# Performance work log

Measured on AMD Instinct MI355X. Metric: run time of the kernel, lower is better.

The kernel has to match this reference:

```python
import jax, jax.numpy as jnp
import numpy as np

N = 10000          # nodes
E = 200000         # edges (avg degree 20)
LAT = 128          # latent dim
NEXP = 8           # experts
NTYPE = 95         # atom types (hard-coded 95x0e in module)
M0, M1, M2 = 128, 64, 32          # node/out irreps muls for l=0,1,2 (dim 480)
E0, E1, E2 = 64, 32, 16           # edge irreps muls (dim 240)
C0, C1, C2 = M0 + E0, M1 + E1, M2 + E2   # concat channels per l
T0 = M0 + M1 + M2                 # gate-input scalars: 128 scalars + 96 gates
AVG_NEIGH = 20.0


def setup_inputs() -> dict:
    key = jax.random.key(0)
    ks = jax.random.split(key, 32)
    r = lambda i, sh: jax.random.normal(ks[i], sh, dtype=jnp.float32)
    return {
        "latents": r(0, (E, LAT)),
        "node_features": r(1, (N, M0 + 3 * M1 + 5 * M2)),
        "edge_features": r(2, (E, E0 + 3 * E1 + 5 * E2)),
        "edge_vector": r(3, (E, 3)),
        "mole_globals": r(4, (LAT,)),
        "wigner_D1": r(5, (E, 3, 3)),
        "wigner_D2": r(6, (E, 5, 5)),
        "node_onehot": jax.nn.one_hot(jax.random.randint(ks[7], (N,), 0, NTYPE), NTYPE, dtype=jnp.float32),
        "Wg": r(8, (LAT, NEXP)),
        "Wm": r(9, (LAT, NEXP)),
        "W0_e": r(10, (NEXP, C0, T0)), "W0_s": r(11, (C0, T0)),
        "W1_e": r(12, (NEXP, C1, M1)), "W1_s": r(13, (C1, M1)),
        "W2_e": r(14, (NEXP, C2, M2)), "W2_s": r(15, (C2, M2)),
        "Wp0": r(16, (M0, M0)), "bp0": jnp.zeros((M0,), jnp.float32),
        "Wp1": r(17, (M1, M1)), "Wp2": r(18, (M2, M2)),
        "Wenv": r(19, (LAT, M0 + M1 + M2)),
        "Woh0": r(20, (M0, NTYPE)), "Woh1": r(21, (M1, NTYPE)), "Woh2": r(22, (M2, NTYPE)),
        "atom_type": jax.random.randint(ks[23], (N,), 0, NTYPE),
        "edge_index": jax.random.randint(ks[24], (2, E), 0, N),
        "active_edges": jnp.arange(E),
    }


def _mix(x, We, Ws, g):
    """Latent(expert)-conditioned per-l channel mixing: y = x @ (sum_e g_e W_e + W_shared).
    Loops over the small fixed expert count; never materializes per-edge weight matrices."""
    xm = x if x.ndim == 3 else x[:, :, None]           # [a, c, m]
    y = jnp.einsum('acm,co->aom', xm, Ws)
    for e in range(NEXP):
        y = y + g[:, e, None, None] * jnp.einsum('acm,co->aom', xm, We[e])
    y = y * float(1.0 / np.sqrt(xm.shape[1]))
    return y[:, :, 0] if x.ndim == 2 else y


def reference(latents, node_features, edge_features, edge_vector, mole_globals,
              wigner_D1, wigner_D2, node_onehot, Wg, Wm,
              W0_e, W0_s, W1_e, W1_s, W2_e, W2_s,
              Wp0, bp0, Wp1, Wp2, Wenv, Woh0, Woh1, Woh2,
              atom_type, edge_index, active_edges):
    edge_center = edge_index[0][active_edges]
    lat = latents[active_edges]
    # gather node features along edges, split irreps blocks
    xn = node_features[edge_center]                         # [Ea, 480]
    n0 = xn[:, :M0]
    n1 = xn[:, M0:M0 + 3 * M1].reshape(-1, M1, 3)
    n2 = xn[:, M0 + 3 * M1:].reshape(-1, M2, 5)
    e0 = edge_features[:, :E0]
    e1 = edge_features[:, E0:E0 + 3 * E1].reshape(-1, E1, 3)
    e2 = edge_features[:, E0 + 3 * E1:].reshape(-1, E2, 5)
    x0 = jnp.concatenate([n0, e0], axis=1)                  # [Ea, C0]
    x1 = jnp.concatenate([n1, e1], axis=1)                  # [Ea, C1, 3]
    x2 = jnp.concatenate([n2, e2], axis=1)                  # [Ea, C2, 5]
    # latent + molecular-global conditioned expert gates
    gates = jax.nn.softmax(lat @ Wg + mole_globals @ Wm, axis=-1)   # [Ea, NEXP]
    # SO(2)-style TP: rotate l>0 blocks into edge frame (Wigner-D), mix channels, rotate back
    x1r = jnp.einsum('amn,acn->acm', wigner_D1, x1)
    x2r = jnp.einsum('amn,acn->acm', wigner_D2, x2)
    t0 = _mix(x0, W0_e, W0_s, gates)                        # [Ea, T0]
    t1 = jnp.einsum('anm,aom->aon', wigner_D1, _mix(x1r, W1_e, W1_s, gates))
    t2 = jnp.einsum('anm,aom->aon', wigner_D2, _mix(x2r, W2_e, W2_s, gates))
    # Gate nonlinearity: silu scalars, sigmoid gates scale l>0 channels
    s = jax.nn.silu(t0[:, :M0])
    v1 = t1 * jax.nn.sigmoid(t0[:, M0:M0 + M1])[:, :, None]
    v2 = t2 * jax.nn.sigmoid(t0[:, M0 + M1:])[:, :, None]
    # lin_post: per-l equivariant linear (bias only on scalars), fan-in normalized
    s = s @ Wp0 * float(1.0 / np.sqrt(M0)) + bp0
    v1 = jnp.einsum('acm,co->aom', v1, Wp1) * float(1.0 / np.sqrt(M1))
    v2 = jnp.einsum('acm,co->aom', v2, Wp2) * float(1.0 / np.sqrt(M2))
    # E3ElementLinear: per-channel weights generated from latents
    w = lat @ Wenv * float(1.0 / np.sqrt(LAT))              # [Ea, M0+M1+M2]
    s = s * w[:, :M0]
    v1 = v1 * w[:, M0:M0 + M1, None]
    v2 = v2 * w[:, M0 + M1:, None]
    # scatter-reduce messages to nodes, normalize by rsqrt(avg_num_neighbors)
    norm = float(1.0 / np.sqrt(AVG_NEIGH))
    o0 = jax.ops.segment_sum(s, edge_center, num_segments=N) * norm
    o1 = jax.ops.segment_sum(v1, edge_center, num_segments=N) * norm
    o2 = jax.ops.segment_sum(v2, edge_center, num_segments=N) * norm
    # residual blend (res_update_params=0 -> u=sigmoid(0)=0.5), identity residual
    u = 0.5
    c_old = float(1.0 / np.sqrt(u * u + 1.0))
    c_new = u * c_old
    h0 = c_old * node_features[:, :M0] + c_new * o0
    h1 = c_old * node_features[:, M0:M0 + 3 * M1].reshape(N, M1, 3) + c_new * o1
    h2 = c_old * node_features[:, M0 + 3 * M1:].reshape(N, M2, 5) + c_new * o2
    # layer-onehot 'uvu' weighted TP with 95x0e, fan-in normalized, added residually
    invs = float(1.0 / np.sqrt(NTYPE))
    h0 = h0 + h0 * (node_onehot @ Woh0.T) * invs
    h1 = h1 + h1 * (node_onehot @ Woh1.T)[:, :, None] * invs
    h2 = h2 + h2 * (node_onehot @ Woh2.T)[:, :, None] * invs
    return jnp.concatenate([h0, h1.reshape(N, 3 * M1), h2.reshape(N, 5 * M2)], axis=1)
```

## Files before the change

kernel.cpp:

```cpp
#include <hip/hip_runtime.h>
#include <math.h>

namespace {

typedef __attribute__((ext_vector_type(8))) short short8;
typedef __attribute__((ext_vector_type(4))) float f32x4;

constexpr int kN   = 10000;
constexpr int kE   = 200000;
constexpr int kNT  = 95;
constexpr int kNFD = 480;

__device__ __forceinline__ ushort bf(float f) {
  union { float f; uint u; } c; c.f = f;
  uint r = c.u + 0x7FFF + ((c.u >> 16) & 1);
  return (ushort)(r >> 16);
}
__device__ __forceinline__ float fb(ushort u) {
  union { uint u; float f; } c; c.u = ((uint)u) << 16;
  return c.f;
}
__device__ __forceinline__ uint pk2(float a, float b) {
  return (uint)bf(a) | ((uint)bf(b) << 16);
}

__device__ __forceinline__ void fastbar() {
  asm volatile("s_waitcnt lgkmcnt(0)" ::: "memory");
  __builtin_amdgcn_s_barrier();
}

__device__ __forceinline__ void packone(int u, const float* We, const float* Ws,
                                        int expStride, int Kreal, int Nstride,
                                        int Nreal, int NT, int NKp, ushort* d) {
  int i = u & 7;
  int lane = (u >> 3) & 63;
  int rest = u >> 9;
  int kc = rest % NKp; rest /= NKp;
  int nt = rest % NT;
  int e  = rest / NT;
  int k = kc*32 + (lane >> 4)*8 + i;
  int n = nt*16 + (lane & 15);
  float v = 0.f;
  if (k < Kreal && n < Nreal) {
    const float* s = (Ws != nullptr && e == 8) ? Ws : (We + (size_t)e*expStride);
    v = s[(size_t)k*Nstride + n];
  }
  d[u] = bf(v);
}

constexpr int PK0   = 0;
constexpr int PK1   = 442368;
constexpr int PK2   = 497664;
constexpr int PKENV = 516096;
constexpr int PKP0  = 544768;
constexpr int PKP1  = 561152;
constexpr int PKP2  = 565248;
constexpr int PKTOT = 566272;

__global__ __launch_bounds__(256)
void pack_k(const float* __restrict__ W0e, const float* __restrict__ W0s,
            const float* __restrict__ W1e, const float* __restrict__ W1s,
            const float* __restrict__ W2e, const float* __restrict__ W2s,
            const float* __restrict__ Wenv, const float* __restrict__ Wp0,
            const float* __restrict__ Wp1, const float* __restrict__ Wp2,
            ushort* __restrict__ dst) {
  int gid = blockIdx.x*256 + threadIdx.x;
  if (gid >= PKTOT) return;
  if (gid < PK1)        packone(gid - PK0,   W0e, W0s, 192*224, 192, 224, 224, 16, 6, dst + PK0);
  else if (gid < PK2)   packone(gid - PK1,   W1e, W1s, 96*64,    96,  64,  64,  4, 3, dst + PK1);
  else if (gid < PKENV) packone(gid - PK2,   W2e, W2s, 48*32,    48,  32,  32,  2, 2, dst + PK2);
  else if (gid < PKP0)  packone(gid - PKENV, Wenv, nullptr, 0,  128, 224, 224, 14, 4, dst + PKENV);
  else if (gid < PKP1)  packone(gid - PKP0,  Wp0, nullptr, 0,   128, 128, 128,  8, 4, dst + PKP0);
  else if (gid < PKP2)  packone(gid - PKP1,  Wp1, nullptr, 0,    64,  64,  64,  4, 2, dst + PKP1);
  else                  packone(gid - PKP2,  Wp2, nullptr, 0,    32,  32,  32,  2, 1, dst + PKP2);
}

__global__ __launch_bounds__(64)
void mgl_k(const float* __restrict__ mgv, const float* __restrict__ Wm,
           float* __restrict__ mgl) {
  int x = threadIdx.x;
  if (x < 8) {
    float s = 0.f;
    for (int l = 0; l < 128; ++l) s += mgv[l]*Wm[l*8 + x];
    mgl[x] = s;
  }
}

__global__ __launch_bounds__(256)
void hist_k(const int* __restrict__ eidx, const int* __restrict__ act,
            int* __restrict__ counts) {
  int e = blockIdx.x*256 + threadIdx.x;
  if (e < kE) atomicAdd(&counts[eidx[act[e]]], 1);
}

__global__ __launch_bounds__(256)
void scan_k(const int* __restrict__ counts, int* __restrict__ rowptr,
            int* __restrict__ cursor) {
  __shared__ int part[256];
  const int t = threadIdx.x;
  const int start = t*40;
  int local = 0;
  for (int i = 0; i < 40; ++i) {
    int idx = start + i;
    if (idx < kN) local += counts[idx];
  }
  part[t] = local;
  __syncthreads();
  for (int ofs = 1; ofs < 256; ofs <<= 1) {
    int v = (t >= ofs) ? part[t - ofs] : 0;
    __syncthreads();
    part[t] += v;
    __syncthreads();
  }
  int run = part[t] - local;
  for (int i = 0; i < 40; ++i) {
    int idx = start + i;
    if (idx < kN) {
      rowptr[idx] = run;
      cursor[idx] = run;
      run += counts[idx];
    }
  }
  if (t == 255) rowptr[kN] = run;
}

__global__ __launch_bounds__(256)
void scatter_k(const int* __restrict__ eidx, const int* __restrict__ act,
               int* __restrict__ cursor, int* __restrict__ elist) {
  int e = blockIdx.x*256 + threadIdx.x;
  if (e < kE) {
    int n = eidx[act[e]];
    int pos = atomicAdd(&cursor[n], 1);
    elist[pos] = e;
  }
}

__global__ __launch_bounds__(256)
void prep_k(const float* __restrict__ latents, const float* __restrict__ nodef,
            const float* __restrict__ edgef, const float* __restrict__ mgl,
            const float* __restrict__ D1, const float* __restrict__ D2,
            const float* __restrict__ Wg,
            const int* __restrict__ eidx, const int* __restrict__ act,
            float* __restrict__ coefg,
            ushort* __restrict__ x0, ushort* __restrict__ x1r,
            ushort* __restrict__ x2r) {
  __shared__ int aidl[32], cenl[32];
  const int tid = threadIdx.x;
  const int base = blockIdx.x*32;

  if (tid < 32) {
    int a = act[base + tid];
    aidl[tid] = a;
    cenl[tid] = eidx[a];
  }
  __syncthreads();

  {
    int e = tid >> 3, x = tid & 7;
    const float* lat = latents + (size_t)aidl[e]*128;
    float s = mgl[x];
    for (int l = 0; l < 128; ++l) s += lat[l]*Wg[l*8 + x];
    float mx = s;
    mx = fmaxf(mx, __shfl_xor(mx, 1));
    mx = fmaxf(mx, __shfl_xor(mx, 2));
    mx = fmaxf(mx, __shfl_xor(mx, 4));
    float ex = __expf(s - mx);
    float sm = ex;
    sm += __shfl_xor(sm, 1);
    sm += __shfl_xor(sm, 2);
    sm += __shfl_xor(sm, 4);
    size_t a = base + e;
    coefg[a*9 + x] = ex/sm;
    if (x == 0) coefg[a*9 + 8] = 1.f;
  }

  for (int u = tid; u < 32*24; u += 256) {
    int e = u/24, g = u - e*24;
    int c0 = g*8;
    size_t a = base + e;
    const float* s = (g < 16) ? (nodef + (size_t)cenl[e]*kNFD + c0)
                              : (edgef + a*240 + (c0 - 128));
    float4 f0 = *(const float4*)s;
    float4 f1 = *(const float4*)(s + 4);
    uint4 o;
    o.x = pk2(f0.x, f0.y); o.y = pk2(f0.z, f0.w);
    o.z = pk2(f1.x, f1.y); o.w = pk2(f1.z, f1.w);
    *(uint4*)(x0 + a*192 + c0) = o;
  }

  for (int u = tid; u < 32*36; u += 256) {
    int e = u/36, r = u - e*36;
    int mm = r/12, g = r - mm*12;
    int c0 = g*8;
    size_t a = base + e;
    const float* dd = D1 + a*9 + mm*3;
    const float* s = (g < 8) ? (nodef + (size_t)cenl[e]*kNFD + 128 + c0*3)
                             : (edgef + a*240 + 64 + (c0 - 64)*3);
    float ld[24];
    #pragma unroll
    for (int q = 0; q < 6; ++q)
      *(float4*)(ld + q*4) = *(const float4*)(s + q*4);
    float d0 = dd[0], d1 = dd[1], d2 = dd[2];
    float ov[8];
    #pragma unroll
    for (int j = 0; j < 8; ++j)
      ov[j] = d0*ld[3*j] + d1*ld[3*j + 1] + d2*ld[3*j + 2];
    uint4 o;
    o.x = pk2(ov[0], ov[1]); o.y = pk2(ov[2], ov[3]);
    o.z = pk2(ov[4], ov[5]); o.w = pk2(ov[6], ov[7]);
    *(uint4*)(x1r + (a*3 + mm)*96 + c0) = o;
  }

  for (int u = tid; u < 32*40; u += 256) {
    int e = u/40, r = u - e*40;
    int mm = r >> 3, g = r & 7;
    int c0 = g*8;
    size_t a = base + e;
    uint4 o = {0u,0u,0u,0u};
    if (g < 6) {
      const float* dd = D2 + a*25 + mm*5;
      const float* s = (g < 4) ? (nodef + (size_t)cenl[e]*kNFD + 320 + c0*5)
                               : (edgef + a*240 + 160 + (c0 - 32)*5);
      float ld[40];
      #pragma unroll
      for (int q = 0; q < 10; ++q)
        *(float4*)(ld + q*4) = *(const float4*)(s + q*4);
      float d0 = dd[0], d1 = dd[1], d2 = dd[2], d3 = dd[3], d4 = dd[4];
      float ov[8];
      #pragma unroll
      for (int j = 0; j < 8; ++j)
        ov[j] = d0*ld[5*j] + d1*ld[5*j+1] + d2*ld[5*j+2] + d3*ld[5*j+3] + d4*ld[5*j+4];
      o.x = pk2(ov[0], ov[1]); o.y = pk2(ov[2], ov[3]);
      o.z = pk2(ov[4], ov[5]); o.w = pk2(ov[6], ov[7]);
    }
    *(uint4*)(x2r + (a*5 + mm)*64 + c0) = o;
  }
}

constexpr int gemm_smbytes(int K1, int NK, int N, int NEXP) {
  int LDA = K1 + 8;
  int NT = N/16;
  int a = 128*LDA*2;
  int b = NT*NK*1024;
  int u = a > b ? a : b;
  return u + (NEXP > 1 ? 128*NEXP*4 : 0);
}

template<int DIV, int K1, int NK, int N, int NEXP, int EPI, bool AF32>
__global__ __launch_bounds__(512)
void gemm_k(const ushort* __restrict__ A, const float* __restrict__ Af,
            const int* __restrict__ ridx, int strideA,
            const ushort* __restrict__ Bpk, const float* __restrict__ coefg,
            int rowsReal, float norm,
            ushort* __restrict__ outbf, const float* __restrict__ bias,
            const ushort* __restrict__ wenvbf, int WCOL) {
  constexpr int NT  = N/16;
  constexpr int CTW = NT/2;
  constexpr int LDA = K1 + 8;
  constexpr int ABYTES = 128*LDA*2;
  constexpr int BBYTES = NT*NK*1024;
  constexpr int UNI = (ABYTES > BBYTES) ? ABYTES : BBYTES;

  extern __shared__ char smraw[];
  ushort* Asm = (ushort*)smraw;
  float* coefsm = (float*)(smraw + UNI);

  const int tid = threadIdx.x;
  const int row0 = blockIdx.x*128;

  constexpr int C8 = K1/8;
  for (int u = tid; u < 128*C8; u += 512) {
    int r = u / C8, c8 = u - r*C8;
    int gr = row0 + r;
    uint4 v = {0u,0u,0u,0u};
    if (gr < rowsReal) {
      if constexpr (AF32) {
        const float* s = Af + (size_t)(ridx ? ridx[gr] : gr)*strideA + c8*8;
        float4 f0 = *(const float4*)s;
        float4 f1 = *(const float4*)(s + 4);
        v.x = pk2(f0.x, f0.y); v.y = pk2(f0.z, f0.w);
        v.z = pk2(f1.x, f1.y); v.w = pk2(f1.z, f1.w);
      } else {
        v = *(const uint4*)(A + (size_t)gr*strideA + c8*8);
      }
    }
    *(uint4*)(&Asm[r*LDA + c8*8]) = v;
  }
  if constexpr (NEXP > 1) {
    for (int u = tid; u < 128*NEXP; u += 512) {
      int r = u / NEXP, e = u - r*NEXP;
      int a = (row0 + r)/DIV;
      coefsm[r*NEXP + e] = coefg[(size_t)a*NEXP + e];
    }
  }
  __syncthreads();

  const int lane = tid & 63, wid = tid >> 6;
  const int cg = wid & 1, rg = wid >> 1;
  const int rbase = rg*32;
  const int lrow = lane & 15, lkb = lane >> 4;

  short8 af[2][NK];
  #pragma unroll
  for (int rt = 0; rt < 2; ++rt)
    #pragma unroll
    for (int kc = 0; kc < NK; ++kc)
      af[rt][kc] = *(const short8*)(&Asm[(rbase + rt*16 + lrow)*LDA + kc*32 + lkb*8]);

  f32x4 acc[2][CTW];
  #pragma unroll
  for (int rt = 0; rt < 2; ++rt)
    #pragma unroll
    for (int ct = 0; ct < CTW; ++ct)
      acc[rt][ct] = f32x4{0.f,0.f,0.f,0.f};

  __syncthreads();

  union BU { uint4 u; short8 s; };
  uint4* Bsm4 = (uint4*)smraw;
  const uint4* Bg4 = (const uint4*)Bpk;

  for (int e = 0; e < NEXP; ++e) {
    for (int u = tid; u < NT*NK*64; u += 512)
      Bsm4[u] = Bg4[(size_t)e*(NT*NK*64) + u];
    __syncthreads();

    if constexpr (NEXP > 1) {
      float cf[2][4];
      #pragma unroll
      for (int rt = 0; rt < 2; ++rt)
        #pragma unroll
        for (int q = 0; q < 4; ++q)
          cf[rt][q] = coefsm[(rbase + rt*16 + lkb*4 + q)*NEXP + e];
      #pragma unroll
      for (int ct = 0; ct < CTW; ++ct) {
        int nt = cg*CTW + ct;
        f32x4 z[2];
        z[0] = f32x4{0.f,0.f,0.f,0.f};
        z[1] = f32x4{0.f,0.f,0.f,0.f};
        #pragma unroll
        for (int kc = 0; kc < NK; ++kc) {
          BU b; b.u = Bsm4[(nt*NK + kc)*64 + lane];
          z[0] = __builtin_amdgcn_mfma_f32_16x16x32_bf16(af[0][kc], b.s, z[0], 0, 0, 0);
          z[1] = __builtin_amdgcn_mfma_f32_16x16x32_bf16(af[1][kc], b.s, z[1], 0, 0, 0);
        }
        #pragma unroll
        for (int q = 0; q < 4; ++q) {
          acc[0][ct][q] += cf[0][q]*z[0][q];
          acc[1][ct][q] += cf[1][q]*z[1][q];
        }
      }
    } else {
      #pragma unroll
      for (int ct = 0; ct < CTW; ++ct) {
        int nt = cg*CTW + ct;
        #pragma unroll
        for (int kc = 0; kc < NK; ++kc) {
          BU b; b.u = Bsm4[(nt*NK + kc)*64 + lane];
          acc[0][ct] = __builtin_amdgcn_mfma_f32_16x16x32_bf16(af[0][kc], b.s, acc[0][ct], 0, 0, 0);
          acc[1][ct] = __builtin_amdgcn_mfma_f32_16x16x32_bf16(af[1][kc], b.s, acc[1][ct], 0, 0, 0);
        }
      }
    }
    __syncthreads();
  }

  #pragma unroll
  for (int rt = 0; rt < 2; ++rt) {
    #pragma unroll
    for (int ct = 0; ct < CTW; ++ct) {
      #pragma unroll
      for (int q = 0; q < 4; ++q) {
        int gr = row0 + rbase + rt*16 + lkb*4 + q;
        if (gr >= rowsReal) continue;
        int o = (cg*CTW + ct)*16 + lrow;
        float val = acc[rt][ct][q]*norm;
        if constexpr (EPI == 0) {
          outbf[(size_t)gr*N + o] = bf(val);
        } else if constexpr (EPI == 1) {
          float av = (o < 128) ? (val/(1.f + __expf(-val)))
                               : (1.f/(1.f + __expf(-val)));
          outbf[(size_t)gr*N + o] = bf(av);
        } else {
          int a = gr/DIV;
          if (bias != nullptr) val += bias[o];
          float w = fb(wenvbf[(size_t)a*224 + WCOL + o]);
          val *= w*0.22360679774997896f;
          outbf[(size_t)gr*N + o] = bf(val);
        }
      }
    }
  }
}

template<int L>
__global__ __launch_bounds__(512)
void pv_k(const ushort* __restrict__ y, const ushort* __restrict__ t0act,
          const float* __restrict__ Dm, const ushort* __restrict__ Bpk,
          int rowsReal, float norm, const ushort* __restrict__ wenvbf,
          ushort* __restrict__ peout) {
  constexpr int DIV = (L == 1) ? 3 : 5;
  constexpr int K1  = (L == 1) ? 64 : 32;
  constexpr int NK  = K1/32;
  constexpr int N   = K1;
  constexpr int NT  = N/16;
  constexpr int CTW = NT/2;
  constexpr int LDA = K1 + 8;
  constexpr int WCOL = (L == 1) ? 128 : 192;
  constexpr int DSTR = (L == 1) ? 9 : 25;
  constexpr int ABYTES = 128*LDA*2;
  constexpr int BBYTES = NT*NK*1024;
  constexpr int UNI = (ABYTES > BBYTES) ? ABYTES : BBYTES;

  extern __shared__ char smraw[];
  ushort* Asm = (ushort*)smraw;

  const int tid = threadIdx.x;
  const int row0 = blockIdx.x*128;

  constexpr int C8 = K1/8;
  for (int u = tid; u < 128*C8; u += 512) {
    int r = u / C8, c8 = u - r*C8;
    int c0 = c8*8;
    int gr = row0 + r;
    uint4 v = {0u,0u,0u,0u};
    if (gr < rowsReal) {
      int a = gr/DIV, n = gr - a*DIV;
      const float* dd = Dm + (size_t)a*DSTR + n*DIV;
      short8 gt = *(const short8*)(t0act + (size_t)a*224 + WCOL + c0);
      float ov[8];
      if constexpr (L == 1) {
        short8 m0 = *(const short8*)(y + ((size_t)a*3 + 0)*64 + c0);
        short8 m1 = *(const short8*)(y + ((size_t)a*3 + 1)*64 + c0);
        short8 m2 = *(const short8*)(y + ((size_t)a*3 + 2)*64 + c0);
        float d0 = dd[0], d1 = dd[1], d2 = dd[2];
        #pragma unroll
        for (int j = 0; j < 8; ++j) {
          float s = d0*fb((ushort)m0[j]) + d1*fb((ushort)m1[j]) + d2*fb((ushort)m2[j]);
          ov[j] = s*fb((ushort)gt[j]);
        }
      } else {
        short8 m0 = *(const short8*)(y + ((size_t)a*5 + 0)*32 + c0);
        short8 m1 = *(const short8*)(y + ((size_t)a*5 + 1)*32 + c0);
        short8 m2 = *(const short8*)(y + ((size_t)a*5 + 2)*32 + c0);
        short8 m3 = *(const short8*)(y + ((size_t)a*5 + 3)*32 + c0);
        short8 m4 = *(const short8*)(y + ((size_t)a*5 + 4)*32 + c0);
        float d0 = dd[0], d1 = dd[1], d2 = dd[2], d3 = dd[3], d4 = dd[4];
        #pragma unroll
        for (int j = 0; j < 8; ++j) {
          float s = d0*fb((ushort)m0[j]) + d1*fb((ushort)m1[j])
                  + d2*fb((ushort)m2[j]) + d3*fb((ushort)m3[j])
                  + d4*fb((ushort)m4[j]);
          ov[j] = s*fb((ushort)gt[j]);
        }
      }
      v.x = pk2(ov[0], ov[1]); v.y = pk2(ov[2], ov[3]);
      v.z = pk2(ov[4], ov[5]); v.w = pk2(ov[6], ov[7]);
    }
    *(uint4*)(&Asm[r*LDA + c0]) = v;
  }
  __syncthreads();

  const int lane = tid & 63, wid = tid >> 6;
  const int cg = wid & 1, rg = wid >> 1;
  const int rbase = rg*32;
  const int lrow = lane & 15, lkb = lane >> 4;

  short8 af[2][NK];
  #pragma unroll
  for (int rt = 0; rt < 2; ++rt)
    #pragma unroll
    for (int kc = 0; kc < NK; ++kc)
      af[rt][kc] = *(const short8*)(&Asm[(rbase + rt*16 + lrow)*LDA + kc*32 + lkb*8]);

  f32x4 acc[2][CTW];
  #pragma unroll
  for (int rt = 0; rt < 2; ++rt)
    #pragma unroll
    for (int ct = 0; ct < CTW; ++ct)
      acc[rt][ct] = f32x4{0.f,0.f,0.f,0.f};

  __syncthreads();

  union BU { uint4 u; short8 s; };
  uint4* Bsm4 = (uint4*)smraw;
  const uint4* Bg4 = (const uint4*)Bpk;

  for (int u = tid; u < NT*NK*64; u += 512)
    Bsm4[u] = Bg4[u];
  __syncthreads();

  #pragma unroll
  for (int ct = 0; ct < CTW; ++ct) {
    int nt = cg*CTW + ct;
    #pragma unroll
    for (int kc = 0; kc < NK; ++kc) {
      BU b; b.u = Bsm4[(nt*NK + kc)*64 + lane];
      acc[0][ct] = __builtin_amdgcn_mfma_f32_16x16x32_bf16(af[0][kc], b.s, acc[0][ct], 0, 0, 0);
      acc[1][ct] = __builtin_amdgcn_mfma_f32_16x16x32_bf16(af[1][kc], b.s, acc[1][ct], 0, 0, 0);
    }
  }

  #pragma unroll
  for (int rt = 0; rt < 2; ++rt) {
    #pragma unroll
    for (int ct = 0; ct < CTW; ++ct) {
      #pragma unroll
      for (int q = 0; q < 4; ++q) {
        int gr = row0 + rbase + rt*16 + lkb*4 + q;
        if (gr >= rowsReal) continue;
        int o = (cg*CTW + ct)*16 + lrow;
        int a = gr/DIV;
        float val = acc[rt][ct][q]*norm;
        float w = fb(wenvbf[(size_t)a*224 + WCOL + o]);
        val *= w*0.22360679774997896f;
        peout[(size_t)gr*N + o] = bf(val);
      }
    }
  }
}

constexpr int T0SMB = 55808;

template<int C>
__device__ __forceinline__ void t0_phase(int e, int tid, int lane, int cg,
                                         int rbase, int lkb,
                                         const short8 (&af)[2][6],
                                         f32x4 (&acc)[2][7],
                                         const float* coefsm,
                                         uint4* Bsm4, const uint4* Bg4,
                                         uint4& rg0, uint4& rg1, uint4& rg2) {
  fastbar();
  const bool hasNext = !(e == 8 && C == 3);
  if (hasNext) {
    int ne = e + (C == 3 ? 1 : 0);
    int nc = (C + 1) & 3;
    const uint4* s = Bg4 + (size_t)ne*6144 + (size_t)nc*1536;
    rg0 = s[tid]; rg1 = s[tid + 512]; rg2 = s[tid + 1024];
  }
  float cf[2][4];
  #pragma unroll
  for (int rt = 0; rt < 2; ++rt)
    #pragma unroll
    for (int q = 0; q < 4; ++q)
      cf[rt][q] = coefsm[(rbase + rt*16 + lkb*4 + q)*9 + e];
  union BU { uint4 u; short8 s; };
  const uint4* bb = Bsm4 + (C & 1)*1536;
  {
    f32x4 z0 = {0.f,0.f,0.f,0.f}, z1 = {0.f,0.f,0.f,0.f};
    #pragma unroll
    for (int kc = 0; kc < 6; ++kc) {
      BU b; b.u = bb[(cg*6 + kc)*64 + lane];
      z0 = __builtin_amdgcn_mfma_f32_16x16x32_bf16(af[0][kc], b.s, z0, 0, 0, 0);
      z1 = __builtin_amdgcn_mfma_f32_16x16x32_bf16(af[1][kc], b.s, z1, 0, 0, 0);
    }
    #pragma unroll
    for (int q = 0; q < 4; ++q) {
      acc[0][2*C][q] += cf[0][q]*z0[q];
      acc[1][2*C][q] += cf[1][q]*z1[q];
    }
  }
  if constexpr (2*C + 1 < 7) {
    f32x4 z0 = {0.f,0.f,0.f,0.f}, z1 = {0.f,0.f,0.f,0.f};
    #pragma unroll
    for (int kc = 0; kc < 6; ++kc) {
      BU b; b.u = bb[((2 + cg)*6 + kc)*64 + lane];
      z0 = __builtin_amdgcn_mfma_f32_16x16x32_bf16(af[0][kc], b.s, z0, 0, 0, 0);
      z1 = __builtin_amdgcn_mfma_f32_16x16x32_bf16(af[1][kc], b.s, z1, 0, 0, 0);
    }
    #pragma unroll
    for (int q = 0; q < 4; ++q) {
      acc[0][2*C + 1][q] += cf[0][q]*z0[q];
      acc[1][2*C + 1][q] += cf[1][q]*z1[q];
    }
  }
  fastbar();
  if (hasNext) {
    uint4* d = Bsm4 + ((C + 1) & 1)*1536;
    d[tid] = rg0; d[tid + 512] = rg1; d[tid + 1024] = rg2;
  }
}

__global__ __launch_bounds__(512, 2)
void t0c_k(const ushort* __restrict__ A, const ushort* __restrict__ Bpk,
           const ushort* __restrict__ Bp0, const float* __restrict__ coefg,
           const float* __restrict__ bp0f, const ushort* __restrict__ wenvbf,
           ushort* __restrict__ t0act, ushort* __restrict__ pe0) {
  extern __shared__ char smraw[];
  ushort* Asm = (ushort*)smraw;
  float* coefsm = (float*)(smraw + 51200);
  uint4* Bsm4 = (uint4*)smraw;
  const uint4* Bg4 = (const uint4*)Bpk;

  const int tid = threadIdx.x;
  const int row0 = blockIdx.x*128;

  for (int u = tid; u < 128*24; u += 512) {
    int r = u/24, c8 = u - r*24;
    int gr = row0 + r;
    uint4 v = {0u,0u,0u,0u};
    if (gr < kE) v = *(const uint4*)(A + (size_t)gr*192 + c8*8);
    *(uint4*)(&Asm[r*200 + c8*8]) = v;
  }
  for (int u = tid; u < 128*9; u += 512) {
    int r = u/9, e = u - r*9;
    coefsm[r*9 + e] = coefg[(size_t)(row0 + r)*9 + e];
  }
  __syncthreads();

  const int lane = tid & 63, wid = tid >> 6;
  const int cg = wid & 1, rg = wid >> 1;
  const int rbase = rg*32;
  const int lrow = lane & 15, lkb = lane >> 4;

  short8 af[2][6];
  #pragma unroll
  for (int rt = 0; rt < 2; ++rt)
    #pragma unroll
    for (int kc = 0; kc < 6; ++kc)
      af[rt][kc] = *(const short8*)(&Asm[(rbase + rt*16 + lrow)*200 + kc*32 + lkb*8]);

  f32x4 acc[2][7];
  #pragma unroll
  for (int rt = 0; rt < 2; ++rt)
    #pragma unroll
    for (int ct = 0; ct < 7; ++ct)
      acc[rt][ct] = f32x4{0.f,0.f,0.f,0.f};

  __syncthreads();

  uint4 rg0, rg1, rg2;
  { const uint4* s = Bg4; rg0 = s[tid]; rg1 = s[tid + 512]; rg2 = s[tid + 1024]; }
  { uint4* d = Bsm4;      d[tid] = rg0; d[tid + 512] = rg1; d[tid + 1024] = rg2; }

  for (int e = 0; e < 9; ++e) {
    t0_phase<0>(e, tid, lane, cg, rbase, lkb, af, acc, coefsm, Bsm4, Bg4, rg0, rg1, rg2);
    t0_phase<1>(e, tid, lane, cg, rbase, lkb, af, acc, coefsm, Bsm4, Bg4, rg0, rg1, rg2);
    t0_phase<2>(e, tid, lane, cg, rbase, lkb, af, acc, coefsm, Bsm4, Bg4, rg0, rg1, rg2);
    t0_phase<3>(e, tid, lane, cg, rbase, lkb, af, acc, coefsm, Bsm4, Bg4, rg0, rg1, rg2);
  }

  ushort* A2 = (ushort*)smraw;
  #pragma unroll
  for (int rt = 0; rt < 2; ++rt) {
    #pragma unroll
    for (int ct = 0; ct < 7; ++ct) {
      int o = (2*ct + cg)*16 + lrow;
      #pragma unroll
      for (int q = 0; q < 4; ++q) {
        int rloc = rbase + rt*16 + lkb*4 + q;
        int gr = row0 + rloc;
        float val = acc[rt][ct][q]*0.07216878364870323f;
        if (o < 128) {
          A2[rloc*136 + o] = bf(val/(1.f + __expf(-val)));
        } else if (gr < kE) {
          t0act[(size_t)gr*224 + o] = bf(1.f/(1.f + __expf(-val)));
        }
      }
    }
  }
  fastbar();

  short8 af2[2][4];
  #pragma unroll
  for (int rt = 0; rt < 2; ++rt)
    #pragma unroll
    for (int kc = 0; kc < 4; ++kc)
      af2[rt][kc] = *(const short8*)(&A2[(rbase + rt*16 + lrow)*136 + kc*32 + lkb*8]);

  union BU { uint4 u; short8 s; };
  const uint4* Bg0 = (const uint4*)Bp0;
  f32x4 acc2[2][4];
  #pragma unroll
  for (int rt = 0; rt < 2; ++rt)
    #pragma unroll
    for (int ct = 0; ct < 4; ++ct)
      acc2[rt][ct] = f32x4{0.f,0.f,0.f,0.f};

  #pragma unroll
  for (int ct = 0; ct < 4; ++ct) {
    int nt = cg*4 + ct;
    #pragma unroll
    for (int kc = 0; kc < 4; ++kc) {
      BU b; b.u = Bg0[(nt*4 + kc)*64 + lane];
      acc2[0][ct] = __builtin_amdgcn_mfma_f32_16x16x32_bf16(af2[0][kc], b.s, acc2[0][ct], 0, 0, 0);
      acc2[1][ct] = __builtin_amdgcn_mfma_f32_16x16x32_bf16(af2[1][kc], b.s, acc2[1][ct], 0, 0, 0);
    }
  }

  #pragma unroll
  for (int rt = 0; rt < 2; ++rt) {
    #pragma unroll
    for (int ct = 0; ct < 4; ++ct) {
      int o = (cg*4 + ct)*16 + lrow;
      float bia = bp0f[o];
      #pragma unroll
      for (int q = 0; q < 4; ++q) {
        int gr = row0 + rbase + rt*16 + lkb*4 + q;
        if (gr >= kE) continue;
        float v = acc2[rt][ct][q]*0.08838834764831845f + bia;
        v *= fb(wenvbf[(size_t)gr*224 + o])*0.22360679774997896f;
        pe0[(size_t)gr*128 + o] = bf(v);
      }
    }
  }
}

constexpr int ych_smbytes(int K1, int NK, int NT) {
  int a = 128*(K1 + 8)*2;
  int b = 2*NT*NK*1024;
  int u = a > b ? a : b;
  return u + 128*9*4;
}

template<int DIV, int K1, int NK, int NT>
__global__ __launch_bounds__(512, 2)
void ychunk_k(const ushort* __restrict__ A, const ushort* __restrict__ Bpk,
              const float* __restrict__ coefg, int rowsReal, float norm,
              ushort* __restrict__ outbf) {
  constexpr int CTW = NT/2;
  constexpr int N   = NT*16;
  constexpr int LDA = K1 + 8;
  constexpr int ABYTES = 128*LDA*2;
  constexpr int BBYTES = 2*NT*NK*1024;
  constexpr int UNI = (ABYTES > BBYTES) ? ABYTES : BBYTES;
  constexpr int NB4 = NT*NK*64;

  extern __shared__ char smraw[];
  ushort* Asm = (ushort*)smraw;
  float* coefsm = (float*)(smraw + UNI);
  uint4* Bsm4 = (uint4*)smraw;
  const uint4* Bg4 = (const uint4*)Bpk;

  const int tid = threadIdx.x;
  const int row0 = blockIdx.x*128;

  constexpr int C8 = K1/8;
  for (int u = tid; u < 128*C8; u += 512) {
    int r = u / C8, c8 = u - r*C8;
    int gr = row0 + r;
    uint4 v = {0u,0u,0u,0u};
    if (gr < rowsReal) v = *(const uint4*)(A + (size_t)gr*K1 + c8*8);
    *(uint4*)(&Asm[r*LDA + c8*8]) = v;
  }
  for (int u = tid; u < 128*9; u += 512) {
    int r = u/9, e = u - r*9;
    int a = (row0 + r)/DIV;
    coefsm[r*9 + e] = coefg[(size_t)a*9 + e];
  }
  __syncthreads();

  const int lane = tid & 63, wid = tid >> 6;
  const int cg = wid & 1, rg = wid >> 1;
  const int rbase = rg*32;
  const int lrow = lane & 15, lkb = lane >> 4;

  short8 af[2][NK];
  #pragma unroll
  for (int rt = 0; rt < 2; ++rt)
    #pragma unroll
    for (int kc = 0; kc < NK; ++kc)
      af[rt][kc] = *(const short8*)(&Asm[(rbase + rt*16 + lrow)*LDA + kc*32 + lkb*8]);

  f32x4 acc[2][CTW];
  #pragma unroll
  for (int rt = 0; rt < 2; ++rt)
    #pragma unroll
    for (int ct = 0; ct < CTW; ++ct)
      acc[rt][ct] = f32x4{0.f,0.f,0.f,0.f};

  __syncthreads();

  union BU { uint4 u; short8 s; };
  uint4 pf0, pf1;

  if (tid < NB4) pf0 = Bg4[tid];
  if constexpr (NB4 > 512) { if (tid + 512 < NB4) pf1 = Bg4[tid + 512]; }
  if (tid < NB4) Bsm4[tid] = pf0;
  if constexpr (NB4 > 512) { if (tid + 512 < NB4) Bsm4[tid + 512] = pf1; }

  for (int e = 0; e < 9; ++e) {
    fastbar();
    if (e + 1 < 9) {
      const uint4* s = Bg4 + (size_t)(e + 1)*NB4;
      if (tid < NB4) pf0 = s[tid];
      if constexpr (NB4 > 512) { if (tid + 512 < NB4) pf1 = s[tid + 512]; }
    }
    float cf[2][4];
    #pragma unroll
    for (int rt = 0; rt < 2; ++rt)
      #pragma unroll
      for (int q = 0; q < 4; ++q)
        cf[rt][q] = coefsm[(rbase + rt*16 + lkb*4 + q)*9 + e];
    const uint4* bb = Bsm4 + (e & 1)*NB4;
    #pragma unroll
    for (int ct = 0; ct < CTW; ++ct) {
      int nt = cg*CTW + ct;
      f32x4 z0 = {0.f,0.f,0.f,0.f}, z1 = {0.f,0.f,0.f,0.f};
      #pragma unroll
      for (int kc = 0; kc < NK; ++kc) {
        BU b; b.u = bb[(nt*NK + kc)*64 + lane];
        z0 = __builtin_amdgcn_mfma_f32_16x16x32_bf16(af[0][kc], b.s, z0, 0, 0, 0);
        z1 = __builtin_amdgcn_mfma_f32_16x16x32_bf16(af[1][kc], b.s, z1, 0, 0, 0);
      }
      #pragma unroll
      for (int q = 0; q < 4; ++q) {
        acc[0][ct][q] += cf[0][q]*z0[q];
        acc[1][ct][q] += cf[1][q]*z1[q];
      }
    }
    fastbar();
    if (e + 1 < 9) {
      uint4* d = Bsm4 + ((e + 1) & 1)*NB4;
      if (tid < NB4) d[tid] = pf0;
      if constexpr (NB4 > 512) { if (tid + 512 < NB4) d[tid + 512] = pf1; }
    }
  }

  #pragma unroll
  for (int rt = 0; rt < 2; ++rt) {
    #pragma unroll
    for (int ct = 0; ct < CTW; ++ct) {
      #pragma unroll
      for (int q = 0; q < 4; ++q) {
        int gr = row0 + rbase + rt*16 + lkb*4 + q;
        if (gr >= rowsReal) continue;
        int o = (cg*CTW + ct)*16 + lrow;
        outbf[(size_t)gr*N + o] = bf(acc[rt][ct][q]*norm);
      }
    }
  }
}

__global__ __launch_bounds__(256)
void gather_k(const float* __restrict__ nodef, const float* __restrict__ onehot,
              const float* __restrict__ Woh0, const float* __restrict__ Woh1,
              const float* __restrict__ Woh2,
              const int* __restrict__ rowptr, const int* __restrict__ elist,
              const ushort* __restrict__ pe0, const ushort* __restrict__ pe1,
              const ushort* __restrict__ pe2, float* __restrict__ out) {
  __shared__ int tn;
  const int n = blockIdx.x;
  const int t = threadIdx.x;
  if (t < kNT && onehot[(size_t)n*kNT + t] > 0.5f) tn = t;
  __syncthreads();
  const int ty = tn;
  const int r0 = rowptr[n], r1 = rowptr[n + 1];
  const float c_old = 0.8944271909999159f;
  const float c_new = 0.4472135954999579f;
  const float invs  = 0.10259783520851541f;

  for (int j = t; j < kNFD; j += 256) {
    int kind, row_m, col;
    if (j < 128)       { kind = 0; row_m = 0; col = j; }
    else if (j < 320)  { int jj = j - 128; col = jj/3; row_m = jj - col*3; kind = 1; }
    else               { int jj = j - 320; col = jj/5; row_m = jj - col*5; kind = 2; }

    float s = 0.f;
    for (int d = r0; d < r1; ++d) {
      int e = elist[d];
      ushort v;
      if (kind == 0)      v = pe0[(size_t)e*128 + col];
      else if (kind == 1) v = pe1[((size_t)e*3 + row_m)*64 + col];
      else                v = pe2[((size_t)e*5 + row_m)*32 + col];
      s += fb(v);
    }

    size_t idx = (size_t)n*kNFD + j;
    float h = c_old*nodef[idx] + c_new*s;
    float f;
    if (j < 128)      f = Woh0[j*kNT + ty];
    else if (j < 320) f = Woh1[((j - 128)/3)*kNT + ty];
    else              f = Woh2[((j - 320)/5)*kNT + ty];
    out[idx] = h*(1.f + f*invs);
  }
}

constexpr size_t OFF_CNT  = 0;
constexpr size_t OFF_CUR  = 40000;
constexpr size_t OFF_RP   = 80000;
constexpr size_t OFF_EL   = 120064;
constexpr size_t OFF_PACK = 1000000;
constexpr size_t OFF_COEF = 19200000;
constexpr size_t OFF_MGL  = 26402304;
constexpr size_t OFF_X0   = 27202560;
constexpr size_t OFF_X1R  = 104027136;
constexpr size_t OFF_PE0  = 168031232;
constexpr size_t OFF_X2R  = 219264000;
constexpr size_t OFF_WENV = 347272192;
constexpr size_t OFF_T0A  = 436900864;
constexpr size_t OFF_Y1   = 526529536;
constexpr size_t OFF_Y2   = 603354112;

}

extern "C" void kernel_launch(void* const* d_in, const int* in_sizes, int n_in,
                              void* d_out, int out_size, void* d_ws, size_t ws_size,
                              hipStream_t stream) {
  (void)in_sizes; (void)n_in; (void)out_size; (void)ws_size;
  const float* latents = (const float*)d_in[0];
  const float* nodef   = (const float*)d_in[1];
  const float* edgef   = (const float*)d_in[2];
  const float* mg      = (const float*)d_in[4];
  const float* D1      = (const float*)d_in[5];
  const float* D2      = (const float*)d_in[6];
  const float* onehot  = (const float*)d_in[7];
  const float* Wg      = (const float*)d_in[8];
  const float* Wm      = (const float*)d_in[9];
  const float* W0e     = (const float*)d_in[10];
  const float* W0s     = (const float*)d_in[11];
  const float* W1e     = (const float*)d_in[12];
  const float* W1s     = (const float*)d_in[13];
  const float* W2e     = (const float*)d_in[14];
  const float* W2s     = (const float*)d_in[15];
  const float* Wp0     = (const float*)d_in[16];
  const float* bp0     = (const float*)d_in[17];
  const float* Wp1     = (const float*)d_in[18];
  const float* Wp2     = (const float*)d_in[19];
  const float* Wenv    = (const float*)d_in[20];
  const float* Woh0    = (const float*)d_in[21];
  const float* Woh1    = (const float*)d_in[22];
  const float* Woh2    = (const float*)d_in[23];
  const int* eidx      = (const int*)d_in[25];
  const int* act       = (const int*)d_in[26];

  char* ws = (char*)d_ws;
  int*    cnt   = (int*)(ws + OFF_CNT);
  int*    cur   = (int*)(ws + OFF_CUR);
  int*    rp    = (int*)(ws + OFF_RP);
  int*    el    = (int*)(ws + OFF_EL);
  ushort* pk    = (ushort*)(ws + OFF_PACK);
  float*  coef  = (float*)(ws + OFF_COEF);
  float*  mgl   = (float*)(ws + OFF_MGL);
  ushort* x0    = (ushort*)(ws + OFF_X0);
  ushort* x1r   = (ushort*)(ws + OFF_X1R);
  ushort* x2r   = (ushort*)(ws + OFF_X2R);
  ushort* wenv  = (ushort*)(ws + OFF_WENV);
  ushort* t0act = (ushort*)(ws + OFF_T0A);
  ushort* y1    = (ushort*)(ws + OFF_Y1);
  ushort* y2    = (ushort*)(ws + OFF_Y2);
  ushort* pe0   = (ushort*)(ws + OFF_PE0);
  ushort* pe1   = (ushort*)(ws + OFF_X2R);
  ushort* pe2   = (ushort*)(ws + OFF_Y1);
  float*  out   = (float*)d_out;

  hipMemsetAsync(cnt, 0, kN*sizeof(int), stream);
  hist_k<<<(kE + 255)/256, 256, 0, stream>>>(eidx, act, cnt);
  scan_k<<<1, 256, 0, stream>>>(cnt, rp, cur);
  scatter_k<<<(kE + 255)/256, 256, 0, stream>>>(eidx, act, cur, el);

  pack_k<<<(PKTOT + 255)/256, 256, 0, stream>>>(W0e, W0s, W1e, W1s, W2e, W2s,
                                                Wenv, Wp0, Wp1, Wp2, pk);
  mgl_k<<<1, 64, 0, stream>>>(mg, Wm, mgl);

  prep_k<<<kE/32, 256, 0, stream>>>(latents, nodef, edgef, mgl, D1, D2, Wg,
                                    eidx, act, coef, x0, x1r, x2r);

  {
    auto kp = gemm_k<1,128,4,224,1,0,true>;
    int smb = gemm_smbytes(128,4,224,1);
    hipFuncSetAttribute((const void*)kp, hipFuncAttributeMaxDynamicSharedMemorySize, smb);
    kp<<<1563, 512, smb, stream>>>(
        nullptr, latents, act, 128, pk + PKENV, nullptr, kE, 0.08838834764831845f,
        wenv, nullptr, nullptr, 0);
  }
  {
    auto kp = ychunk_k<3,96,3,4>;
    int smb = ych_smbytes(96,3,4);
    hipFuncSetAttribute((const void*)kp, hipFuncAttributeMaxDynamicSharedMemorySize, smb);
    kp<<<4688, 512, smb, stream>>>(
        x1r, pk + PK1, coef, 3*kE, 0.10206207261596577f, y1);
  }
  {
    auto kp = ychunk_k<5,64,2,2>;
    int smb = ych_smbytes(64,2,2);
    hipFuncSetAttribute((const void*)kp, hipFuncAttributeMaxDynamicSharedMemorySize, smb);
    kp<<<7813, 512, smb, stream>>>(
        x2r, pk + PK2, coef, 5*kE, 0.14433756729740643f, y2);
  }

  {
    hipFuncSetAttribute((const void*)t0c_k,
                        hipFuncAttributeMaxDynamicSharedMemorySize, T0SMB);
    t0c_k<<<1563, 512, T0SMB, stream>>>(x0, pk + PK0, pk + PKP0, coef,
                                        bp0, wenv, t0act, pe0);
  }

  {
    auto kp = pv_k<1>;
    int smb = gemm_smbytes(64,2,64,1);
    hipFuncSetAttribute((const void*)kp, hipFuncAttributeMaxDynamicSharedMemorySize, smb);
    kp<<<4688, 512, smb, stream>>>(
        y1, t0act, D1, pk + PKP1, 3*kE, 0.125f, wenv, pe1);
  }
  {
    auto kp = pv_k<2>;
    int smb = gemm_smbytes(32,1,32,1);
    hipFuncSetAttribute((const void*)kp, hipFuncAttributeMaxDynamicSharedMemorySize, smb);
    kp<<<7813, 512, smb, stream>>>(
        y2, t0act, D2, pk + PKP2, 5*kE, 0.17677669529663687f, wenv, pe2);
  }

  gather_k<<<kN, 256, 0, stream>>>(nodef, onehot, Woh0, Woh1, Woh2,
                                   rp, el, pe0, pe1, pe2, out);
}
```

Baseline: 1.313 ms.

## Fuse input gather and Wigner rotation into GEMM A-tile loaders

```diff
diff --git a/kernel.cpp b/kernel.cpp
--- a/kernel.cpp
+++ b/kernel.cpp
@@ -136,105 +136,32 @@
 }
 
 __global__ __launch_bounds__(256)
-void prep_k(const float* __restrict__ latents, const float* __restrict__ nodef,
-            const float* __restrict__ edgef, const float* __restrict__ mgl,
-            const float* __restrict__ D1, const float* __restrict__ D2,
-            const float* __restrict__ Wg,
-            const int* __restrict__ eidx, const int* __restrict__ act,
-            float* __restrict__ coefg,
-            ushort* __restrict__ x0, ushort* __restrict__ x1r,
-            ushort* __restrict__ x2r) {
-  __shared__ int aidl[32], cenl[32];
+void coef_k(const float* __restrict__ latents, const float* __restrict__ mgl,
+            const float* __restrict__ Wg, const int* __restrict__ act,
+            float* __restrict__ coefg) {
+  __shared__ int aidl[32];
   const int tid = threadIdx.x;
   const int base = blockIdx.x*32;
 
-  if (tid < 32) {
-    int a = act[base + tid];
-    aidl[tid] = a;
-    cenl[tid] = eidx[a];
-  }
-  __syncthreads();
-
-  {
-    int e = tid >> 3, x = tid & 7;
-    const float* lat = latents + (size_t)aidl[e]*128;
-    float s = mgl[x];
-    for (int l = 0; l < 128; ++l) s += lat[l]*Wg[l*8 + x];
-    float mx = s;
-    mx = fmaxf(mx, __shfl_xor(mx, 1));
-    mx = fmaxf(mx, __shfl_xor(mx, 2));
-    mx = fmaxf(mx, __shfl_xor(mx, 4));
-    float ex = __expf(s - mx);
-    float sm = ex;
-    sm += __shfl_xor(sm, 1);
-    sm += __shfl_xor(sm, 2);
-    sm += __shfl_xor(sm, 4);
-    size_t a = base + e;
-    coefg[a*9 + x] = ex/sm;
-    if (x == 0) coefg[a*9 + 8] = 1.f;
-  }
-
-  for (int u = tid; u < 32*24; u += 256) {
-    int e = u/24, g = u - e*24;
-    int c0 = g*8;
-    size_t a = base + e;
-    const float* s = (g < 16) ? (nodef + (size_t)cenl[e]*kNFD + c0)
-                              : (edgef + a*240 + (c0 - 128));
-    float4 f0 = *(const float4*)s;
-    float4 f1 = *(const float4*)(s + 4);
-    uint4 o;
-    o.x = pk2(f0.x, f0.y); o.y = pk2(f0.z, f0.w);
-    o.z = pk2(f1.x, f1.y); o.w = pk2(f1.z, f1.w);
-    *(uint4*)(x0 + a*192 + c0) = o;
-  }
-
-  for (int u = tid; u < 32*36; u += 256) {
-    int e = u/36, r = u - e*36;
-    int mm = r/12, g = r - mm*12;
-    int c0 = g*8;
-    size_t a = base + e;
-    const float* dd = D1 + a*9 + mm*3;
-    const float* s = (g < 8) ? (nodef + (size_t)cenl[e]*kNFD + 128 + c0*3)
-                             : (edgef + a*240 + 64 + (c0 - 64)*3);
-    float ld[24];
-    #pragma unroll
-    for (int q = 0; q < 6; ++q)
-      *(float4*)(ld + q*4) = *(const float4*)(s + q*4);
-    float d0 = dd[0], d1 = dd[1], d2 = dd[2];
-    float ov[8];
-    #pragma unroll
-    for (int j = 0; j < 8; ++j)
-      ov[j] = d0*ld[3*j] + d1*ld[3*j + 1] + d2*ld[3*j + 2];
-    uint4 o;
-    o.x = pk2(ov[0], ov[1]); o.y = pk2(ov[2], ov[3]);
-    o.z = pk2(ov[4], ov[5]); o.w = pk2(ov[6], ov[7]);
-    *(uint4*)(x1r + (a*3 + mm)*96 + c0) = o;
-  }
-
-  for (int u = tid; u < 32*40; u += 256) {
-    int e = u/40, r = u - e*40;
-    int mm = r >> 3, g = r & 7;
-    int c0 = g*8;
-    size_t a = base + e;
-    uint4 o = {0u,0u,0u,0u};
-    if (g < 6) {
-      const float* dd = D2 + a*25 + mm*5;
-      const float* s = (g < 4) ? (nodef + (size_t)cenl[e]*kNFD + 320 + c0*5)
-                               : (edgef + a*240 + 160 + (c0 - 32)*5);
-      float ld[40];
-      #pragma unroll
-      for (int q = 0; q < 10; ++q)
-        *(float4*)(ld + q*4) = *(const float4*)(s + q*4);
-      float d0 = dd[0], d1 = dd[1], d2 = dd[2], d3 = dd[3], d4 = dd[4];
-      float ov[8];
-      #pragma unroll
-      for (int j = 0; j < 8; ++j)
-        ov[j] = d0*ld[5*j] + d1*ld[5*j+1] + d2*ld[5*j+2] + d3*ld[5*j+3] + d4*ld[5*j+4];
-      o.x = pk2(ov[0], ov[1]); o.y = pk2(ov[2], ov[3]);
-      o.z = pk2(ov[4], ov[5]); o.w = pk2(ov[6], ov[7]);
-    }
-    *(uint4*)(x2r + (a*5 + mm)*64 + c0) = o;
-  }
+  if (tid < 32) aidl[tid] = act[base + tid];
+  __syncthreads();
+
+  int e = tid >> 3, x = tid & 7;
+  const float* lat = latents + (size_t)aidl[e]*128;
+  float s = mgl[x];
+  for (int l = 0; l < 128; ++l) s += lat[l]*Wg[l*8 + x];
+  float mx = s;
+  mx = fmaxf(mx, __shfl_xor(mx, 1));
+  mx = fmaxf(mx, __shfl_xor(mx, 2));
+  mx = fmaxf(mx, __shfl_xor(mx, 4));
+  float ex = __expf(s - mx);
+  float sm = ex;
+  sm += __shfl_xor(sm, 1);
+  sm += __shfl_xor(sm, 2);
+  sm += __shfl_xor(sm, 4);
+  size_t a = base + e;
+  coefg[a*9 + x] = ex/sm;
+  if (x == 0) coefg[a*9 + 8] = 1.f;
 }
 
 constexpr int gemm_smbytes(int K1, int NK, int N, int NEXP) {
@@ -408,9 +335,6 @@
   constexpr int LDA = K1 + 8;
   constexpr int WCOL = (L == 1) ? 128 : 192;
   constexpr int DSTR = (L == 1) ? 9 : 25;
-  constexpr int ABYTES = 128*LDA*2;
-  constexpr int BBYTES = NT*NK*1024;
-  constexpr int UNI = (ABYTES > BBYTES) ? ABYTES : BBYTES;
 
   extern __shared__ char smraw[];
   ushort* Asm = (ushort*)smraw;
@@ -582,11 +506,14 @@
 }
 
 __global__ __launch_bounds__(512, 2)
-void t0c_k(const ushort* __restrict__ A, const ushort* __restrict__ Bpk,
-           const ushort* __restrict__ Bp0, const float* __restrict__ coefg,
-           const float* __restrict__ bp0f, const ushort* __restrict__ wenvbf,
+void t0c_k(const float* __restrict__ nodef, const float* __restrict__ edgef,
+           const int* __restrict__ eidx, const int* __restrict__ act,
+           const ushort* __restrict__ Bpk, const ushort* __restrict__ Bp0,
+           const float* __restrict__ coefg, const float* __restrict__ bp0f,
+           const ushort* __restrict__ wenvbf,
            ushort* __restrict__ t0act, ushort* __restrict__ pe0) {
   extern __shared__ char smraw[];
+  __shared__ int cenl[128];
   ushort* Asm = (ushort*)smraw;
   float* coefsm = (float*)(smraw + 51200);
   uint4* Bsm4 = (uint4*)smraw;
@@ -595,12 +522,26 @@
   const int tid = threadIdx.x;
   const int row0 = blockIdx.x*128;
 
+  if (tid < 128) {
+    int gr = row0 + tid;
+    cenl[tid] = (gr < kE) ? eidx[act[gr]] : 0;
+  }
+  __syncthreads();
+
   for (int u = tid; u < 128*24; u += 512) {
-    int r = u/24, c8 = u - r*24;
+    int r = u/24, g = u - r*24;
+    int c0 = g*8;
     int gr = row0 + r;
     uint4 v = {0u,0u,0u,0u};
-    if (gr < kE) v = *(const uint4*)(A + (size_t)gr*192 + c8*8);
-    *(uint4*)(&Asm[r*200 + c8*8]) = v;
+    if (gr < kE) {
+      const float* s = (g < 16) ? (nodef + (size_t)cenl[r]*kNFD + c0)
+                                : (edgef + (size_t)gr*240 + (c0 - 128));
+      float4 f0 = *(const float4*)s;
+      float4 f1 = *(const float4*)(s + 4);
+      v.x = pk2(f0.x, f0.y); v.y = pk2(f0.z, f0.w);
+      v.z = pk2(f1.x, f1.y); v.w = pk2(f1.z, f1.w);
+    }
+    *(uint4*)(&Asm[r*200 + c0]) = v;
   }
   for (int u = tid; u < 128*9; u += 512) {
     int r = u/9, e = u - r*9;
@@ -713,9 +654,11 @@
   return u + 128*9*4;
 }
 
-template<int DIV, int K1, int NK, int NT>
+template<int DIV, int K1, int NK, int NT, int FUSE>
 __global__ __launch_bounds__(512, 2)
-void ychunk_k(const ushort* __restrict__ A, const ushort* __restrict__ Bpk,
+void ychunk_k(const float* __restrict__ nodef, const float* __restrict__ edgef,
+              const float* __restrict__ Dm, const int* __restrict__ eidx,
+              const int* __restrict__ act, const ushort* __restrict__ Bpk,
               const float* __restrict__ coefg, int rowsReal, float norm,
               ushort* __restrict__ outbf) {
   constexpr int CTW = NT/2;
@@ -725,6 +668,7 @@
   constexpr int BBYTES = 2*NT*NK*1024;
   constexpr int UNI = (ABYTES > BBYTES) ? ABYTES : BBYTES;
   constexpr int NB4 = NT*NK*64;
+  constexpr int DSTR = (FUSE == 1) ? 9 : 25;
 
   extern __shared__ char smraw[];
   ushort* Asm = (ushort*)smraw;
@@ -738,10 +682,46 @@
   constexpr int C8 = K1/8;
   for (int u = tid; u < 128*C8; u += 512) {
     int r = u / C8, c8 = u - r*C8;
+    int c0 = c8*8;
     int gr = row0 + r;
     uint4 v = {0u,0u,0u,0u};
-    if (gr < rowsReal) v = *(const uint4*)(A + (size_t)gr*K1 + c8*8);
-    *(uint4*)(&Asm[r*LDA + c8*8]) = v;
+    if (gr < rowsReal) {
+      int a = gr/DIV, mm = gr - a*DIV;
+      int cen = eidx[act[a]];
+      const float* dd = Dm + (size_t)a*DSTR + mm*DIV;
+      if constexpr (FUSE == 1) {
+        const float* s = (c8 < 8) ? (nodef + (size_t)cen*kNFD + 128 + c0*3)
+                                  : (edgef + (size_t)a*240 + 64 + (c0 - 64)*3);
+        float ld[24];
+        #pragma unroll
+        for (int q = 0; q < 6; ++q)
+          *(float4*)(ld + q*4) = *(const float4*)(s + q*4);
+        float d0 = dd[0], d1 = dd[1], d2 = dd[2];
+        float ov[8];
+        #pragma unroll
+        for (int j = 0; j < 8; ++j)
+          ov[j] = d0*ld[3*j] + d1*ld[3*j + 1] + d2*ld[3*j + 2];
+        v.x = pk2(ov[0], ov[1]); v.y = pk2(ov[2], ov[3]);
+        v.z = pk2(ov[4], ov[5]); v.w = pk2(ov[6], ov[7]);
+      } else {
+        if (c0 < 48) {
+          const float* s = (c0 < 32) ? (nodef + (size_t)cen*kNFD + 320 + c0*5)
+                                     : (edgef + (size_t)a*240 + 160 + (c0 - 32)*5);
+          float ld[40];
+          #pragma unroll
+          for (int q = 0; q < 10; ++q)
+            *(float4*)(ld + q*4) = *(const float4*)(s + q*4);
+          float d0 = dd[0], d1 = dd[1], d2 = dd[2], d3 = dd[3], d4 = dd[4];
+          float ov[8];
+          #pragma unroll
+          for (int j = 0; j < 8; ++j)
+            ov[j] = d0*ld[5*j] + d1*ld[5*j+1] + d2*ld[5*j+2] + d3*ld[5*j+3] + d4*ld[5*j+4];
+          v.x = pk2(ov[0], ov[1]); v.y = pk2(ov[2], ov[3]);
+          v.z = pk2(ov[4], ov[5]); v.w = pk2(ov[6], ov[7]);
+        }
+      }
+    }
+    *(uint4*)(&Asm[r*LDA + c0]) = v;
   }
   for (int u = tid; u < 128*9; u += 512) {
     int r = u/9, e = u - r*9;
@@ -883,8 +863,6 @@
 constexpr size_t OFF_PACK = 1000000;
 constexpr size_t OFF_COEF = 19200000;
 constexpr size_t OFF_MGL  = 26402304;
-constexpr size_t OFF_X0   = 27202560;
-constexpr size_t OFF_X1R  = 104027136;
 constexpr size_t OFF_PE0  = 168031232;
 constexpr size_t OFF_X2R  = 219264000;
 constexpr size_t OFF_WENV = 347272192;
@@ -932,9 +910,6 @@
   ushort* pk    = (ushort*)(ws + OFF_PACK);
   float*  coef  = (float*)(ws + OFF_COEF);
   float*  mgl   = (float*)(ws + OFF_MGL);
-  ushort* x0    = (ushort*)(ws + OFF_X0);
-  ushort* x1r   = (ushort*)(ws + OFF_X1R);
-  ushort* x2r   = (ushort*)(ws + OFF_X2R);
   ushort* wenv  = (ushort*)(ws + OFF_WENV);
   ushort* t0act = (ushort*)(ws + OFF_T0A);
   ushort* y1    = (ushort*)(ws + OFF_Y1);
@@ -953,8 +928,7 @@
                                                 Wenv, Wp0, Wp1, Wp2, pk);
   mgl_k<<<1, 64, 0, stream>>>(mg, Wm, mgl);
 
-  prep_k<<<kE/32, 256, 0, stream>>>(latents, nodef, edgef, mgl, D1, D2, Wg,
-                                    eidx, act, coef, x0, x1r, x2r);
+  coef_k<<<kE/32, 256, 0, stream>>>(latents, mgl, Wg, act, coef);
 
   {
     auto kp = gemm_k<1,128,4,224,1,0,true>;
@@ -965,24 +939,27 @@
         wenv, nullptr, nullptr, 0);
   }
   {
-    auto kp = ychunk_k<3,96,3,4>;
+    auto kp = ychunk_k<3,96,3,4,1>;
     int smb = ych_smbytes(96,3,4);
     hipFuncSetAttribute((const void*)kp, hipFuncAttributeMaxDynamicSharedMemorySize, smb);
     kp<<<4688, 512, smb, stream>>>(
-        x1r, pk + PK1, coef, 3*kE, 0.10206207261596577f, y1);
+        nodef, edgef, D1, eidx, act, pk + PK1, coef, 3*kE,
+        0.10206207261596577f, y1);
   }
   {
-    auto kp = ychunk_k<5,64,2,2>;
+    auto kp = ychunk_k<5,64,2,2,2>;
     int smb = ych_smbytes(64,2,2);
     hipFuncSetAttribute((const void*)kp, hipFuncAttributeMaxDynamicSharedMemorySize, smb);
     kp<<<7813, 512, smb, stream>>>(
-        x2r, pk + PK2, coef, 5*kE, 0.14433756729740643f, y2);
+        nodef, edgef, D2, eidx, act, pk + PK2, coef, 5*kE,
+        0.14433756729740643f, y2);
   }
 
   {
     hipFuncSetAttribute((const void*)t0c_k,
                         hipFuncAttributeMaxDynamicSharedMemorySize, T0SMB);
-    t0c_k<<<1563, 512, T0SMB, stream>>>(x0, pk + PK0, pk + PKP0, coef,
+    t0c_k<<<1563, 512, T0SMB, stream>>>(nodef, edgef, eidx, act,
+                                        pk + PK0, pk + PKP0, coef,
                                         bp0, wenv, t0act, pe0);
   }
 
```

After: 1.272 ms. 1.03x faster.
